# Kernel optimization log

Measured on AMD Instinct MI355X. Metric: run time of the kernel, lower is better.

The kernel has to match this reference:

```python
import jax, jax.numpy as jnp
import numpy as np

N = 65536
H = 1024
E = 3  # experts: SwishGLU, GEGLU, ReGLU


def setup_inputs() -> dict:
    key = jax.random.key(0)
    ks = jax.random.split(key, 10)
    s = 1.0 / np.sqrt(H)
    return {
        "x": jax.random.normal(ks[0], (N, H), jnp.float32),
        "W1": jax.random.normal(ks[1], (E, H, H), jnp.float32) * s,
        "b1": jax.random.normal(ks[2], (E, H), jnp.float32) * s,
        "W2": jax.random.normal(ks[3], (E, H, H), jnp.float32) * s,
        "b2": jax.random.normal(ks[4], (E, H), jnp.float32) * s,
        "W3": jax.random.normal(ks[5], (E, H, H), jnp.float32) * s,
        "b3": jax.random.normal(ks[6], (E, H), jnp.float32) * s,
        "Wg": jax.random.normal(ks[7], (H, E), jnp.float32) * s,
        "bg": jax.random.normal(ks[8], (E,), jnp.float32) * s,
        "gumbel_u": jax.random.uniform(ks[9], (N, E), jnp.float32),
    }


def reference(x, W1, b1, W2, b2, W3, b3, Wg, bg, gumbel_u):
    # Gate: hard gumbel-softmax (tau=1, hard=True) with straight-through estimator
    logits = x @ Wg + bg                                   # [N, E]
    u = jnp.clip(gumbel_u, 1e-6, 1.0 - 1e-6)
    g = -jnp.log(-jnp.log(u))                              # Gumbel(0,1) noise
    y_soft = jax.nn.softmax(logits + g, axis=-1)           # [N, E]
    y_hard = jax.nn.one_hot(jnp.argmax(y_soft, axis=-1), E, dtype=x.dtype)
    gate = y_hard + y_soft - jax.lax.stop_gradient(y_soft)  # values == y_hard

    # Dense compute of all three GLU experts (faithful to original module)
    h1 = jnp.einsum('nd,edh->enh', x, W1) + b1[:, None, :]  # [E, N, H]
    h3 = jnp.einsum('nd,edh->enh', x, W3) + b3[:, None, :]  # [E, N, H]
    acts = jnp.stack([
        jax.nn.silu(h1[0]),                       # SwishGLU
        jax.nn.gelu(h1[1], approximate=False),    # GEGLU (exact erf gelu)
        jax.nn.relu(h1[2]),                       # ReGLU
    ], axis=0)                                    # [E, N, H]
    inner = acts * h3                             # [E, N, H]
    out_e = jnp.einsum('end,edh->enh', inner, W2) + b2[:, None, :]  # [E, N, H]

    # Select/mix with (hard) gate weights
    return jnp.einsum('enh,ne->nh', out_e, gate)  # [N, H]
```

## Files before the change

kernel.cpp:

```cpp
#include <hip/hip_runtime.h>
#include <math.h>

#define N_TOK 65536
#define H_DIM 1024

typedef __attribute__((ext_vector_type(8))) short bf16x8;
typedef __attribute__((ext_vector_type(4))) float f32x4;

static const size_t WS_CNT   = 0;
static const size_t WS_OFFS  = 64;
static const size_t WS_PERM  = 128;
static const size_t WS_WT13  = 1ull << 20;
static const size_t WS_WT2   = WS_WT13 + 12582912ull;
static const size_t WS_XB    = 20ull << 20;
static const size_t WS_INNER = WS_XB + 134217728ull;

static __device__ __forceinline__ unsigned short f2bf(float f) {
  union { float f; unsigned int u; } v; v.f = f;
  unsigned int r = v.u + 0x7fffu + ((v.u >> 16) & 1u);
  return (unsigned short)(r >> 16);
}

static __device__ __forceinline__ float fast_exp2(float x) {
  float r; asm("v_exp_f32 %0, %1" : "=v"(r) : "v"(x)); return r;
}
static __device__ __forceinline__ float fast_rcp(float x) {
  float r; asm("v_rcp_f32 %0, %1" : "=v"(r) : "v"(x)); return r;
}

static __device__ __forceinline__ void gload16(const void* g, void* l) {
  __builtin_amdgcn_global_load_lds(
      (const __attribute__((address_space(1))) unsigned int*)g,
      (__attribute__((address_space(3))) unsigned int*)l, 16, 0, 0);
}

static __device__ __forceinline__ void bar() {
  asm volatile("" ::: "memory");
  __builtin_amdgcn_s_barrier();
  asm volatile("" ::: "memory");
}

__global__ void init_kernel(int* cnt) {
  if (threadIdx.x < 4) cnt[threadIdx.x] = 0;
}

__global__ __launch_bounds__(1024) void gate_kernel(
    const float* __restrict__ x, const float* __restrict__ Wg,
    const float* __restrict__ bg, const float* __restrict__ gu,
    unsigned short* __restrict__ xb, int* __restrict__ cnt,
    int* __restrict__ perm)
{
  __shared__ float wg[3072];
  __shared__ int bexp[16];
  for (int i = threadIdx.x; i < 3072; i += 1024) wg[i] = Wg[i];
  __syncthreads();
  const int wave = threadIdx.x >> 6;
  const int lane = threadIdx.x & 63;
  const int n0 = blockIdx.x * 16;
  const int n = n0 + wave;
  const float4* xrow = (const float4*)(x + (size_t)n * H_DIM);
  unsigned short* xbrow = xb + (size_t)n * H_DIM;
  float s0 = 0.f, s1 = 0.f, s2 = 0.f;
#pragma unroll
  for (int j = 0; j < 4; j++) {
    float4 v = xrow[j * 64 + lane];
    int d0 = (j * 64 + lane) * 4;
    const float* w = &wg[d0 * 3];
    s0 += v.x * w[0] + v.y * w[3] + v.z * w[6] + v.w * w[9];
    s1 += v.x * w[1] + v.y * w[4] + v.z * w[7] + v.w * w[10];
    s2 += v.x * w[2] + v.y * w[5] + v.z * w[8] + v.w * w[11];
    uint2 p;
    p.x = (unsigned)f2bf(v.x) | ((unsigned)f2bf(v.y) << 16);
    p.y = (unsigned)f2bf(v.z) | ((unsigned)f2bf(v.w) << 16);
    ((uint2*)xbrow)[j * 64 + lane] = p;
  }
#pragma unroll
  for (int o = 32; o; o >>= 1) {
    s0 += __shfl_xor(s0, o);
    s1 += __shfl_xor(s1, o);
    s2 += __shfl_xor(s2, o);
  }
  if (lane == 0) {
    const float* u = gu + (size_t)n * 3;
    float l[3] = { s0 + bg[0], s1 + bg[1], s2 + bg[2] };
    int best = 0; float bs = -1e30f;
#pragma unroll
    for (int e = 0; e < 3; e++) {
      float uc = fminf(fmaxf(u[e], 1e-6f), 1.f - 1e-6f);
      float g = -logf(-logf(uc));
      float s = l[e] + g;
      if (s > bs) { bs = s; best = e; }
    }
    bexp[wave] = best;
  }
  __syncthreads();
  if (threadIdx.x == 0) {
    int lc[3] = {0, 0, 0};
    int lpos[16];
    for (int w = 0; w < 16; w++) lpos[w] = lc[bexp[w]]++;
    int lbase[3];
    for (int e = 0; e < 3; e++)
      lbase[e] = lc[e] ? atomicAdd(&cnt[e], lc[e]) : 0;
    for (int w = 0; w < 16; w++) {
      int e = bexp[w];
      perm[e * N_TOK + lbase[e] + lpos[w]] = n0 + w;
    }
  }
}

__global__ void offs_kernel(const int* __restrict__ cnt, int* __restrict__ offs) {
  offs[0] = 0; offs[1] = cnt[0]; offs[2] = cnt[0] + cnt[1]; offs[3] = N_TOK;
}

__global__ __launch_bounds__(256) void wcvt_kernel(
    const float* __restrict__ W1, const float* __restrict__ W3,
    const float* __restrict__ W2,
    unsigned short* __restrict__ wt13, unsigned short* __restrict__ wt2)
{
  const int z = blockIdx.z, e = z / 3, m = z % 3;
  const float* src = (m == 0 ? W1 : (m == 1 ? W3 : W2)) + ((size_t)e << 20);
  __shared__ float t[64][33];
  const int h0 = blockIdx.x * 32, d0 = blockIdx.y * 64;
  const int tid = threadIdx.x;
  const int lh = tid & 31, lk = tid >> 5;
#pragma unroll
  for (int j = 0; j < 8; j++)
    t[j * 8 + lk][lh] = src[(size_t)(d0 + j * 8 + lk) * H_DIM + h0 + lh];
  __syncthreads();
  const int h_l = tid >> 3, kc = tid & 7;
  const int h = h0 + h_l;
  unsigned short sv[8];
#pragma unroll
  for (int j = 0; j < 8; j++) sv[j] = f2bf(t[kc * 8 + j][h_l]);
  const int kpos = d0 + ((kc ^ (h & 7)) << 3);
  if (m == 2) {
    *(uint4*)&wt2[((size_t)e << 20) + ((size_t)h << 10) + kpos] = *(const uint4*)sv;
  } else {
    const int nc = ((h >> 4) << 5) + (m << 4) + (h & 15);
    *(uint4*)&wt13[((size_t)e << 21) + ((size_t)nc << 10) + kpos] = *(const uint4*)sv;
  }
}

#define MFMA16(d, bb, aa) d = __builtin_amdgcn_mfma_f32_16x16x32_bf16((bb), (aa), (d), 0, 0, 0)

template<int PH>
__global__ __launch_bounds__(512, 2) void mlp_kernel(
    const unsigned short* __restrict__ A,
    const unsigned short* __restrict__ B,
    const float* __restrict__ bA, const float* __restrict__ bB,
    const int* __restrict__ cnt, const int* __restrict__ offs,
    const int* __restrict__ perm,
    unsigned short* __restrict__ inner, float* __restrict__ out)
{
  constexpr int NXT = (PH == 1) ? 8 : 4;
  const int e = blockIdx.z;
  const int ce = cnt[e];
  const int f = blockIdx.x + NXT * blockIdx.y;
  const int mt = (f & 7) + 8 * ((f >> 3) / NXT);
  const int nt = (f >> 3) % NXT;
  const int m0 = mt << 8;
  if (m0 >= ce) return;
  const int n0 = nt << 8;
  const int oe = offs[e];

  __shared__ short smem[65536];

  const int tid = threadIdx.x;
  const int wid = tid >> 6, lane = tid & 63;
  const int wm = (wid >> 2) * 128, wn = (wid & 3) * 64;
  const int lr = lane & 15, quad = lane >> 4;
  const int xa = lane & 7;
  const int sl = lane >> 3, sc = lane & 7;

  unsigned aoff[4], boff[4];
  int ldsA[4], ldsB[4];
#pragma unroll
  for (int h = 0; h < 2; h++)
#pragma unroll
    for (int si = 0; si < 2; si++) {
      const int hs = h * 2 + si;
      const int rowb = h * 128 + (wid + si * 8) * 8;
      const int r = rowb + sl;
      unsigned arow;
      if constexpr (PH == 1) {
        arow = (unsigned)perm[e * N_TOK + min(m0 + r, ce - 1)];
      } else {
        arow = (unsigned)(oe + min(m0 + r, ce - 1));
      }
      aoff[hs] = (arow << 10) + (unsigned)((sc ^ sl) << 3);
      const unsigned brow = (PH == 1 ? ((unsigned)e << 11) : ((unsigned)e << 10))
                          + (unsigned)(n0 + r);
      boff[hs] = (brow << 10) + (unsigned)(sc << 3);
      ldsA[hs] = rowb * 64;
      ldsB[hs] = 16384 + rowb * 64;
    }

  f32x4 acc[8][4];
#pragma unroll
  for (int i = 0; i < 8; i++)
#pragma unroll
    for (int j = 0; j < 4; j++) acc[i][j] = (f32x4){0.f, 0.f, 0.f, 0.f};

#define ISSA(d, hs, k0) gload16(A + aoff[hs] + (k0), &smem[(d) * 32768 + ldsA[hs]])
#define ISSB(d, hs, k0) gload16(B + boff[hs] + (k0), &smem[(d) * 32768 + ldsB[hs]])
#define LDA_(mi, kx) (*(const bf16x8*)&As[(wm + (mi) * 16 + lr) * 64 + (((((kx) << 2) + quad) ^ xa) << 3)])
#define LDB_(nj, kx) (*(const bf16x8*)&Bs[(wn + (nj) * 16 + lr) * 64 + (((((kx) << 2) + quad) ^ xa) << 3)])

  ISSA(0, 0, 0);  ISSA(0, 1, 0);  ISSA(0, 2, 0);  ISSA(0, 3, 0);
  ISSB(0, 0, 0);  ISSB(0, 1, 0);  ISSB(0, 2, 0);  ISSB(0, 3, 0);
  ISSB(1, 0, 64); ISSB(1, 1, 64); ISSB(1, 2, 64); ISSB(1, 3, 64);
  asm volatile("s_waitcnt vmcnt(4)" ::: "memory");
  bar();

#pragma unroll 2
  for (int tt = 0; tt < 16; tt++) {
    const int cur = tt & 1, nxt = cur ^ 1;
    const short* As = smem + cur * 32768;
    const short* Bs = As + 16384;
    const int k1 = (tt + 1) << 6, k2 = (tt + 2) << 6;
    bf16x8 a0[4][2], a1[4][2], bfr[4][2];

#pragma unroll
    for (int mi = 0; mi < 4; mi++) { a0[mi][0] = LDA_(mi, 0); a0[mi][1] = LDA_(mi, 1); }
#pragma unroll
    for (int nj = 0; nj < 2; nj++) { bfr[nj][0] = LDB_(nj, 0); bfr[nj][1] = LDB_(nj, 1); }
    if (tt < 15) { ISSA(nxt, 0, k1); ISSA(nxt, 1, k1); }
    bar();
    __builtin_amdgcn_s_setprio(1);
#pragma unroll
    for (int kk = 0; kk < 2; kk++)
#pragma unroll
      for (int mi = 0; mi < 4; mi++)
#pragma unroll
        for (int nj = 0; nj < 2; nj++)
          MFMA16(acc[mi][nj], bfr[nj][kk], a0[mi][kk]);
    __builtin_amdgcn_s_setprio(0);
    bar();

#pragma unroll
    for (int nj = 2; nj < 4; nj++) { bfr[nj][0] = LDB_(nj, 0); bfr[nj][1] = LDB_(nj, 1); }
    if (tt < 15) { ISSA(nxt, 2, k1); ISSA(nxt, 3, k1); }
    bar();
    __builtin_amdgcn_s_setprio(1);
#pragma unroll
    for (int kk = 0; kk < 2; kk++)
#pragma unroll
      for (int mi = 0; mi < 4; mi++)
#pragma unroll
        for (int nj = 2; nj < 4; nj++)
          MFMA16(acc[mi][nj], bfr[nj][kk], a0[mi][kk]);
    __builtin_amdgcn_s_setprio(0);
    bar();

#pragma unroll
    for (int mi = 0; mi < 4; mi++) { a1[mi][0] = LDA_(mi + 4, 0); a1[mi][1] = LDA_(mi + 4, 1); }
    if (tt < 14) { ISSB(cur, 0, k2); ISSB(cur, 1, k2); }
    bar();
    __builtin_amdgcn_s_setprio(1);
#pragma unroll
    for (int kk = 0; kk < 2; kk++)
#pragma unroll
      for (int mi = 0; mi < 4; mi++)
#pragma unroll
        for (int nj = 0; nj < 2; nj++)
          MFMA16(acc[mi + 4][nj], bfr[nj][kk], a1[mi][kk]);
    __builtin_amdgcn_s_setprio(0);
    bar();

    if (tt < 14) { ISSB(cur, 2, k2); ISSB(cur, 3, k2); }
    __builtin_amdgcn_s_setprio(1);
#pragma unroll
    for (int kk = 0; kk < 2; kk++)
#pragma unroll
      for (int mi = 0; mi < 4; mi++)
#pragma unroll
        for (int nj = 2; nj < 4; nj++)
          MFMA16(acc[mi + 4][nj], bfr[nj][kk], a1[mi][kk]);
    __builtin_amdgcn_s_setprio(0);
    if (tt < 14)      asm volatile("s_waitcnt vmcnt(4)" ::: "memory");
    else if (tt < 15) asm volatile("s_waitcnt vmcnt(0)" ::: "memory");
    if (tt < 15) bar();
  }

#undef ISSA
#undef ISSB
#undef LDA_
#undef LDB_

  if constexpr (PH == 1) {
    const int colg = (((n0 + wn) >> 5) << 4) + quad * 4;
#pragma unroll
    for (int p = 0; p < 2; p++) {
      const int colb = colg + p * 16;
      const float4 v1 = *(const float4*)&bA[e * H_DIM + colb];
      const float4 v3 = *(const float4*)&bB[e * H_DIM + colb];
#pragma unroll
      for (int mi = 0; mi < 8; mi++) {
        const int rr = m0 + wm + mi * 16 + lr;
        if (rr < ce) {
          unsigned short sv[4];
#pragma unroll
          for (int r = 0; r < 4; r++) {
            const float h1 = acc[mi][2 * p][r]     + ((const float*)&v1)[r];
            const float h3 = acc[mi][2 * p + 1][r] + ((const float*)&v3)[r];
            float a;
            if (e == 0)      a = h1 * fast_rcp(1.f + fast_exp2(h1 * -1.44269504f));
            else if (e == 1) a = 0.5f * h1 * (1.f + erff(h1 * 0.70710678118f));
            else             a = fmaxf(h1, 0.f);
            sv[r] = f2bf(a * h3);
          }
          *(uint2*)&inner[((size_t)(oe + rr) << 10) + colb] = *(const uint2*)sv;
        }
      }
    }
  } else {
#pragma unroll
    for (int nj = 0; nj < 4; nj++) {
      const int colb = n0 + wn + nj * 16 + quad * 4;
      const float4 v2 = *(const float4*)&bA[e * H_DIM + colb];
#pragma unroll
      for (int mi = 0; mi < 8; mi++) {
        const int rr = m0 + wm + mi * 16 + lr;
        if (rr < ce) {
          const int g = perm[e * N_TOK + rr];
          float4 v;
          v.x = acc[mi][nj][0] + v2.x;
          v.y = acc[mi][nj][1] + v2.y;
          v.z = acc[mi][nj][2] + v2.z;
          v.w = acc[mi][nj][3] + v2.w;
          *(float4*)&out[((size_t)g << 10) + colb] = v;
        }
      }
    }
  }
}

extern "C" void kernel_launch(void* const* d_in, const int* in_sizes, int n_in,
                              void* d_out, int out_size, void* d_ws, size_t ws_size,
                              hipStream_t stream)
{
  const float* x  = (const float*)d_in[0];
  const float* W1 = (const float*)d_in[1];
  const float* b1 = (const float*)d_in[2];
  const float* W2 = (const float*)d_in[3];
  const float* b2 = (const float*)d_in[4];
  const float* W3 = (const float*)d_in[5];
  const float* b3 = (const float*)d_in[6];
  const float* Wg = (const float*)d_in[7];
  const float* bg = (const float*)d_in[8];
  const float* gu = (const float*)d_in[9];
  float* out = (float*)d_out;

  char* ws = (char*)d_ws;
  int* cnt  = (int*)(ws + WS_CNT);
  int* offs = (int*)(ws + WS_OFFS);
  int* perm = (int*)(ws + WS_PERM);
  unsigned short* wt13 = (unsigned short*)(ws + WS_WT13);
  unsigned short* wt2  = (unsigned short*)(ws + WS_WT2);
  unsigned short* xb   = (unsigned short*)(ws + WS_XB);
  unsigned short* inner = (unsigned short*)(ws + WS_INNER);

  init_kernel<<<1, 64, 0, stream>>>(cnt);
  gate_kernel<<<N_TOK / 16, 1024, 0, stream>>>(x, Wg, bg, gu, xb, cnt, perm);
  offs_kernel<<<1, 1, 0, stream>>>(cnt, offs);
  wcvt_kernel<<<dim3(32, 16, 9), 256, 0, stream>>>(W1, W3, W2, wt13, wt2);
  mlp_kernel<1><<<dim3(8, 256, 3), 512, 0, stream>>>(
      xb, wt13, b1, b3, cnt, offs, perm, inner, nullptr);
  mlp_kernel<2><<<dim3(4, 256, 3), 512, 0, stream>>>(
      inner, wt2, b2, nullptr, cnt, offs, perm, nullptr, out);
}
```

Before: 1.056 ms.

## Restructure GEMM main loop into two k-halves with fewer barriers

Replaces the four-phase ping-pong loop (interleaved A/B fragment loads, global prefetch issues and barriers per quarter) with two phases per k-tile: load all A/B fragments for k-half 0, run the full 8x4 MFMA block, then repeat for k-half 1, with a single barrier before issuing the B prefetch. This cuts barrier count per iteration and gives larger MFMA bursts, at the cost of more live registers and less fine-grained overlap between LDS reads and MFMA. Separately, the gate kernel transposes Wg in shared memory so each thread reads contiguous float4 weights instead of strided scalars.

```diff
diff --git a/kernel.cpp b/kernel.cpp
--- a/kernel.cpp
+++ b/kernel.cpp
@@ -52,7 +52,8 @@
 {
   __shared__ float wg[3072];
   __shared__ int bexp[16];
-  for (int i = threadIdx.x; i < 3072; i += 1024) wg[i] = Wg[i];
+  for (int i = threadIdx.x; i < 3072; i += 1024)
+    wg[(i % 3) * 1024 + (i / 3)] = Wg[i];
   __syncthreads();
   const int wave = threadIdx.x >> 6;
   const int lane = threadIdx.x & 63;
@@ -65,10 +66,12 @@
   for (int j = 0; j < 4; j++) {
     float4 v = xrow[j * 64 + lane];
     int d0 = (j * 64 + lane) * 4;
-    const float* w = &wg[d0 * 3];
-    s0 += v.x * w[0] + v.y * w[3] + v.z * w[6] + v.w * w[9];
-    s1 += v.x * w[1] + v.y * w[4] + v.z * w[7] + v.w * w[10];
-    s2 += v.x * w[2] + v.y * w[5] + v.z * w[8] + v.w * w[11];
+    float4 a0 = *(const float4*)&wg[d0];
+    float4 a1 = *(const float4*)&wg[1024 + d0];
+    float4 a2 = *(const float4*)&wg[2048 + d0];
+    s0 += v.x * a0.x + v.y * a0.y + v.z * a0.z + v.w * a0.w;
+    s1 += v.x * a1.x + v.y * a1.y + v.z * a1.z + v.w * a1.w;
+    s2 += v.x * a2.x + v.y * a2.y + v.z * a2.z + v.w * a2.w;
     uint2 p;
     p.x = (unsigned)f2bf(v.x) | ((unsigned)f2bf(v.y) << 16);
     p.y = (unsigned)f2bf(v.z) | ((unsigned)f2bf(v.w) << 16);
@@ -218,65 +221,34 @@
     const short* As = smem + cur * 32768;
     const short* Bs = As + 16384;
     const int k1 = (tt + 1) << 6, k2 = (tt + 2) << 6;
-    bf16x8 a0[4][2], a1[4][2], bfr[4][2];
-
-#pragma unroll
-    for (int mi = 0; mi < 4; mi++) { a0[mi][0] = LDA_(mi, 0); a0[mi][1] = LDA_(mi, 1); }
-#pragma unroll
-    for (int nj = 0; nj < 2; nj++) { bfr[nj][0] = LDB_(nj, 0); bfr[nj][1] = LDB_(nj, 1); }
-    if (tt < 15) { ISSA(nxt, 0, k1); ISSA(nxt, 1, k1); }
+    bf16x8 af[8], bf0[4], ag[8], bg1[4];
+
+#pragma unroll
+    for (int mi = 0; mi < 8; mi++) af[mi] = LDA_(mi, 0);
+#pragma unroll
+    for (int nj = 0; nj < 4; nj++) bf0[nj] = LDB_(nj, 0);
+    if (tt < 15) { ISSA(nxt, 0, k1); ISSA(nxt, 1, k1); ISSA(nxt, 2, k1); ISSA(nxt, 3, k1); }
+    __builtin_amdgcn_s_setprio(1);
+#pragma unroll
+    for (int mi = 0; mi < 8; mi++)
+#pragma unroll
+      for (int nj = 0; nj < 4; nj++)
+        MFMA16(acc[mi][nj], bf0[nj], af[mi]);
+    __builtin_amdgcn_s_setprio(0);
+#pragma unroll
+    for (int mi = 0; mi < 8; mi++) ag[mi] = LDA_(mi, 1);
+#pragma unroll
+    for (int nj = 0; nj < 4; nj++) bg1[nj] = LDB_(nj, 1);
+    __builtin_amdgcn_s_setprio(1);
+#pragma unroll
+    for (int mi = 0; mi < 8; mi++)
+#pragma unroll
+      for (int nj = 0; nj < 4; nj++)
+        MFMA16(acc[mi][nj], bg1[nj], ag[mi]);
+    __builtin_amdgcn_s_setprio(0);
+
     bar();
-    __builtin_amdgcn_s_setprio(1);
-#pragma unroll
-    for (int kk = 0; kk < 2; kk++)
-#pragma unroll
-      for (int mi = 0; mi < 4; mi++)
-#pragma unroll
-        for (int nj = 0; nj < 2; nj++)
-          MFMA16(acc[mi][nj], bfr[nj][kk], a0[mi][kk]);
-    __builtin_amdgcn_s_setprio(0);
-    bar();
-
-#pragma unroll
-    for (int nj = 2; nj < 4; nj++) { bfr[nj][0] = LDB_(nj, 0); bfr[nj][1] = LDB_(nj, 1); }
-    if (tt < 15) { ISSA(nxt, 2, k1); ISSA(nxt, 3, k1); }
-    bar();
-    __builtin_amdgcn_s_setprio(1);
-#pragma unroll
-    for (int kk = 0; kk < 2; kk++)
-#pragma unroll
-      for (int mi = 0; mi < 4; mi++)
-#pragma unroll
-        for (int nj = 2; nj < 4; nj++)
-          MFMA16(acc[mi][nj], bfr[nj][kk], a0[mi][kk]);
-    __builtin_amdgcn_s_setprio(0);
-    bar();
-
-#pragma unroll
-    for (int mi = 0; mi < 4; mi++) { a1[mi][0] = LDA_(mi + 4, 0); a1[mi][1] = LDA_(mi + 4, 1); }
-    if (tt < 14) { ISSB(cur, 0, k2); ISSB(cur, 1, k2); }
-    bar();
-    __builtin_amdgcn_s_setprio(1);
-#pragma unroll
-    for (int kk = 0; kk < 2; kk++)
-#pragma unroll
-      for (int mi = 0; mi < 4; mi++)
-#pragma unroll
-        for (int nj = 0; nj < 2; nj++)
-          MFMA16(acc[mi + 4][nj], bfr[nj][kk], a1[mi][kk]);
-    __builtin_amdgcn_s_setprio(0);
-    bar();
-
-    if (tt < 14) { ISSB(cur, 2, k2); ISSB(cur, 3, k2); }
-    __builtin_amdgcn_s_setprio(1);
-#pragma unroll
-    for (int kk = 0; kk < 2; kk++)
-#pragma unroll
-      for (int mi = 0; mi < 4; mi++)
-#pragma unroll
-        for (int nj = 2; nj < 4; nj++)
-          MFMA16(acc[mi + 4][nj], bfr[nj][kk], a1[mi][kk]);
-    __builtin_amdgcn_s_setprio(0);
+    if (tt < 14) { ISSB(cur, 0, k2); ISSB(cur, 1, k2); ISSB(cur, 2, k2); ISSB(cur, 3, k2); }
     if (tt < 14)      asm volatile("s_waitcnt vmcnt(4)" ::: "memory");
     else if (tt < 15) asm volatile("s_waitcnt vmcnt(0)" ::: "memory");
     if (tt < 15) bar();
```

New measurement: 1.070 ms. About the same (+1.3%).
